# Kernel tuning notes

Hardware: AMD Instinct MI355X
Metric: run time of the kernel (lower is better)

Reference implementation:

```python
import jax, jax.numpy as jnp
import numpy as np

EPS = 1e-5

def _ln(x, g, b):
    mu = jnp.mean(x, axis=-1, keepdims=True)
    var = jnp.mean((x - mu) ** 2, axis=-1, keepdims=True)
    return (x - mu) * jax.lax.rsqrt(var + EPS) * g + b

def setup_inputs() -> dict:
    key = jax.random.key(0)
    B, V, I, H = 32, 48, 24, 768
    ks = jax.random.split(key, 10)
    s = 0.02
    return {
        'variables': jax.random.normal(ks[0], (B, V, H), jnp.float32),
        'interventions': jax.random.normal(ks[1], (B, I, H), jnp.float32),
        # variable_encoder: Linear(H,H) + LayerNorm(H)
        'W_enc': jax.random.normal(ks[2], (H, H), jnp.float32) * s,
        'b_enc': jnp.zeros((H,), jnp.float32),
        'g_enc': jnp.ones((H,), jnp.float32),
        'be_enc': jnp.zeros((H,), jnp.float32),
        # graph_generator: Linear(2H,H) + LN(H) + ReLU + Linear(H,1) + Sigmoid
        'Wg1': jax.random.normal(ks[3], (2 * H, H), jnp.float32) * s,
        'bg1': jnp.zeros((H,), jnp.float32),
        'g_g': jnp.ones((H,), jnp.float32),
        'b_g': jnp.zeros((H,), jnp.float32),
        'Wg2': jax.random.normal(ks[4], (H, 1), jnp.float32) * s,
        'bg2': jnp.zeros((1,), jnp.float32),
        # intervention_predictor: Linear(2H,H) + LN(H) + ReLU + Linear(H,H)
        'Wi1': jax.random.normal(ks[5], (2 * H, H), jnp.float32) * s,
        'bi1': jnp.zeros((H,), jnp.float32),
        'g_i': jnp.ones((H,), jnp.float32),
        'b_i': jnp.zeros((H,), jnp.float32),
        'Wi2': jax.random.normal(ks[6], (H, H), jnp.float32) * s,
        'bi2': jnp.zeros((H,), jnp.float32),
    }

def reference(variables, interventions, W_enc, b_enc, g_enc, be_enc,
              Wg1, bg1, g_g, b_g, Wg2, bg2, Wi1, bi1, g_i, b_i, Wi2, bi2):
    H = variables.shape[-1]
    V = variables.shape[1]
    # variable encoder: Linear + LayerNorm + ReLU
    enc = jax.nn.relu(_ln(variables @ W_enc + b_enc, g_enc, be_enc))  # [B,V,H]

    # graph generator over all ordered pairs (i,j): concat([enc_i, enc_j]) @ Wg1
    # split Wg1 so the concat-matmul becomes two small GEMMs + broadcast add
    hi = jnp.einsum('bvh,hk->bvk', enc, Wg1[:H])   # contribution of enc_i
    hj = jnp.einsum('bvh,hk->bvk', enc, Wg1[H:])   # contribution of enc_j
    h = jax.nn.relu(_ln(hi[:, :, None, :] + hj[:, None, :, :] + bg1, g_g, b_g))  # [B,V,V,H]
    score = jax.nn.sigmoid(jnp.squeeze(h @ Wg2, -1) + bg2[0])  # [B,V,V]
    # diagonal (i==j) is never written in the original -> stays zero
    causal_graph = score * (1.0 - jnp.eye(V, dtype=score.dtype))

    # intervention predictor: concat([intervention_i, enc_j]) -> MLP
    ha = jnp.einsum('bih,hk->bik', interventions, Wi1[:H])  # [B,I,H]
    hb = jnp.einsum('bvh,hk->bvk', enc, Wi1[H:])            # [B,V,H]
    h2 = jax.nn.relu(_ln(ha[:, :, None, :] + hb[:, None, :, :] + bi1, g_i, b_i))  # [B,I,V,H]
    effects = h2 @ Wi2 + bi2  # [B,I,V,H]

    return (effects, causal_graph, enc)
```

## Files before the change

kernel.cpp:

```cpp
#include <hip/hip_runtime.h>
#include <math.h>

#define Bp 32
#define Vp 48
#define Ip 24
#define Hp 768
#define EPS 1e-5f

#define EFFECTS_SIZE (Bp*Ip*Vp*Hp)
#define GRAPH_SIZE   (Bp*Vp*Vp)
#define ENC_SIZE     (Bp*Vp*Hp)
#define MS           (Hp*Hp)

typedef __attribute__((ext_vector_type(8))) short short8;
typedef __attribute__((ext_vector_type(4))) float floatx4;
typedef __attribute__((ext_vector_type(2))) float floatx2;
typedef __attribute__((ext_vector_type(4))) unsigned int uintx4;

__device__ __forceinline__ unsigned short f2bf(float f) {
    unsigned int u = __float_as_uint(f);
    u += 0x7fffu + ((u >> 16) & 1u);
    return (unsigned short)(u >> 16);
}
__device__ __forceinline__ unsigned int f2bf2(float a, float b) {
    return (unsigned int)f2bf(a) | ((unsigned int)f2bf(b) << 16);
}

__device__ __forceinline__ uintx4 ln8(floatx4 xa, floatx4 xb, float mu, float rs,
                                      floatx4 ga, floatx4 gb, floatx4 ba, floatx4 bb)
{
    float y0 = fmaxf((xa.x - mu) * rs * ga.x + ba.x, 0.f);
    float y1 = fmaxf((xa.y - mu) * rs * ga.y + ba.y, 0.f);
    float y2 = fmaxf((xa.z - mu) * rs * ga.z + ba.z, 0.f);
    float y3 = fmaxf((xa.w - mu) * rs * ga.w + ba.w, 0.f);
    float y4 = fmaxf((xb.x - mu) * rs * gb.x + bb.x, 0.f);
    float y5 = fmaxf((xb.y - mu) * rs * gb.y + bb.y, 0.f);
    float y6 = fmaxf((xb.z - mu) * rs * gb.z + bb.z, 0.f);
    float y7 = fmaxf((xb.w - mu) * rs * gb.w + bb.w, 0.f);
    uintx4 v;
    v.x = f2bf2(y0, y1); v.y = f2bf2(y2, y3);
    v.z = f2bf2(y4, y5); v.w = f2bf2(y6, y7);
    return v;
}

__global__ __launch_bounds__(256) void pack_weights(
    const float* __restrict__ W_enc, const float* __restrict__ Wg1,
    const float* __restrict__ Wi1, const float* __restrict__ Wi2,
    unsigned short* __restrict__ packed)
{
    const int bid = blockIdx.x;
    const int m = bid / 288;
    const int rem = bid - m * 288;
    const int T = rem / 6;
    const int u = rem - T * 6;
    const float* src;
    switch (m) {
        case 0: src = W_enc; break;
        case 1: src = Wg1; break;
        case 2: src = Wg1 + Hp * Hp; break;
        case 3: src = Wi1 + Hp * Hp; break;
        case 4: src = Wi1; break;
        default: src = Wi2; break;
    }
    unsigned short* dst = packed + (size_t)m * MS;
    const int lane = threadIdx.x & 63;
    const int kq = threadIdx.x >> 6;
    const int col = T * 16 + (lane & 15);
    const int krow0 = (lane >> 4) * 8;
    const int kb = kq + 4 * u;
    unsigned int w[4];
#pragma unroll
    for (int p2 = 0; p2 < 4; ++p2) {
        float f0 = src[(size_t)(kb * 32 + krow0 + 2 * p2)     * Hp + col];
        float f1 = src[(size_t)(kb * 32 + krow0 + 2 * p2 + 1) * Hp + col];
        w[p2] = f2bf2(f0, f1);
    }
    uintx4 v; v.x = w[0]; v.y = w[1]; v.z = w[2]; v.w = w[3];
    *(uintx4*)(dst + ((size_t)(T * 24 + kb) * 64 + lane) * 8) = v;
}

__global__ __launch_bounds__(256) void convert_inputs(
    const float* __restrict__ vars, const float* __restrict__ intv,
    const float* __restrict__ bg1, const float* __restrict__ bi1,
    unsigned short* __restrict__ varb, unsigned short* __restrict__ intvb,
    float* __restrict__ bias2304)
{
    const int p = blockIdx.x * 256 + threadIdx.x;
    const int VPn = ENC_SIZE / 2;
    if (p < VPn) {
        float2 f = ((const float2*)vars)[p];
        ((unsigned int*)varb)[p] = f2bf2(f.x, f.y);
    } else {
        int q = p - VPn;
        float2 f = ((const float2*)intv)[q];
        ((unsigned int*)intvb)[q] = f2bf2(f.x, f.y);
    }
    if (blockIdx.x == 0) {
        for (int t = threadIdx.x; t < 2304; t += 256)
            bias2304[t] = (t < 768) ? 0.0f : (t < 1536 ? bg1[t - 768] : bi1[t - 1536]);
    }
}

__device__ __forceinline__ void gemm32_body(
    unsigned short* Asl,
    const unsigned short* __restrict__ A, const unsigned short* __restrict__ Bpk,
    const float* __restrict__ bias, float* __restrict__ C, int ldc,
    int bx, int by)
{
    const int tid = threadIdx.x, wave = tid >> 6, lane = tid & 63;
    const int m0 = bx * 32;

#pragma unroll
    for (int uu = 0; uu < 12; ++uu) {
        const int s = tid + 256 * uu;
        const int mt = s / 1536;
        const int r2 = s - mt * 1536;
        const int kb = r2 >> 6;
        const int L  = r2 & 63;
        uintx4 v = *(const uintx4*)(A + (size_t)(m0 + mt * 16 + (L & 15)) * Hp
                                      + kb * 32 + (L >> 4) * 8);
        *(uintx4*)(&Asl[((mt * 24 + kb) * 64 + (L ^ (kb & 7))) * 8]) = v;
    }
    __syncthreads();

    const int mrow = lane & 15, kq = lane >> 4;
    const int rot = ((bx * 5 + by) & 7) * 3;
    const int wavep = (wave + bx) & 3;
    const int Tg0 = by * 12 + wavep * 3;
    const unsigned short* Bbase = Bpk + (size_t)Tg0 * 12288 + lane * 8;

    const floatx4 z = {0.f, 0.f, 0.f, 0.f};
    floatx4 acc[2][3];
#pragma unroll
    for (int mt = 0; mt < 2; ++mt)
#pragma unroll
        for (int nt = 0; nt < 3; ++nt) acc[mt][nt] = z;

    short8 bbuf[4][3], abuf[2][2];
#pragma unroll
    for (int d = 0; d < 3; ++d) {
        int kc = d + rot; if (kc >= 24) kc -= 24;
#pragma unroll
        for (int nt = 0; nt < 3; ++nt)
            bbuf[d][nt] = *(const short8*)(Bbase + (size_t)nt * 12288 + kc * 512);
    }
    {
        int kc = rot;
#pragma unroll
        for (int mt = 0; mt < 2; ++mt)
            abuf[0][mt] = *(const short8*)(&Asl[((mt * 24 + kc) * 64 + (lane ^ (kc & 7))) * 8]);
    }

#pragma unroll
    for (int kb = 0; kb < 24; ++kb) {
        if (kb + 3 < 24) {
            int kc = kb + 3 + rot; if (kc >= 24) kc -= 24;
#pragma unroll
            for (int nt = 0; nt < 3; ++nt)
                bbuf[(kb + 3) & 3][nt] =
                    *(const short8*)(Bbase + (size_t)nt * 12288 + kc * 512);
        }
        if (kb + 1 < 24) {
            int kc = kb + 1 + rot; if (kc >= 24) kc -= 24;
#pragma unroll
            for (int mt = 0; mt < 2; ++mt)
                abuf[(kb + 1) & 1][mt] = *(const short8*)(
                    &Asl[((mt * 24 + kc) * 64 + (lane ^ (kc & 7))) * 8]);
        }
        __builtin_amdgcn_s_setprio(1);
#pragma unroll
        for (int mt = 0; mt < 2; ++mt)
#pragma unroll
            for (int nt = 0; nt < 3; ++nt)
                acc[mt][nt] = __builtin_amdgcn_mfma_f32_16x16x32_bf16(
                    abuf[kb & 1][mt], bbuf[kb & 3][nt], acc[mt][nt], 0, 0, 0);
        __builtin_amdgcn_s_setprio(0);
    }

#pragma unroll
    for (int nt = 0; nt < 3; ++nt) {
        const int colg = (Tg0 + nt) * 16 + mrow;
        const float bv = bias ? bias[colg] : 0.0f;
#pragma unroll
        for (int mt = 0; mt < 2; ++mt)
#pragma unroll
            for (int r = 0; r < 4; ++r)
                C[(size_t)(m0 + mt * 16 + kq * 4 + r) * ldc + colg] = acc[mt][nt][r] + bv;
    }
}

__global__ __launch_bounds__(256) void gemm32(
    const unsigned short* __restrict__ A, const unsigned short* __restrict__ Bpk,
    const float* __restrict__ bias, float* __restrict__ C, int ldc)
{
    __shared__ unsigned short Asl[2 * 24 * 64 * 8];
    gemm32_body(Asl, A, Bpk, bias, C, ldc, blockIdx.x, blockIdx.y);
}

__global__ __launch_bounds__(256) void gemm32_pair(
    const unsigned short* __restrict__ A1, const unsigned short* __restrict__ B1,
    const float* __restrict__ bias1, float* __restrict__ C1,
    const unsigned short* __restrict__ A2, const unsigned short* __restrict__ B2,
    float* __restrict__ C2)
{
    __shared__ unsigned short Asl[2 * 24 * 64 * 8];
    if (blockIdx.y < 4) {
        gemm32_body(Asl, A1, B1, bias1, C1, Hp, blockIdx.x, blockIdx.y);
    } else {
        if (blockIdx.x >= 24) return;
        gemm32_body(Asl, A2, B2, nullptr, C2, Hp, blockIdx.x, blockIdx.y - 4);
    }
}

__global__ __launch_bounds__(256) void ln_relu(
    const float* __restrict__ pre, const float* __restrict__ g,
    const float* __restrict__ be, float* __restrict__ encf,
    unsigned short* __restrict__ encb)
{
    const int wave = threadIdx.x >> 6, lane = threadIdx.x & 63;
    const int row = blockIdx.x * 4 + wave;
    const float2* rp = (const float2*)(pre + (size_t)row * Hp);
    float2 x[6]; float s = 0.f, q = 0.f;
#pragma unroll
    for (int c = 0; c < 6; ++c) {
        x[c] = rp[lane + 64 * c];
        s += x[c].x + x[c].y;
        q += x[c].x * x[c].x + x[c].y * x[c].y;
    }
#pragma unroll
    for (int m = 1; m < 64; m <<= 1) { s += __shfl_xor(s, m, 64); q += __shfl_xor(q, m, 64); }
    const float mu = s * (1.0f / Hp);
    const float var = q * (1.0f / Hp) - mu * mu;
    const float rs = rsqrtf(var + EPS);
    floatx2* of = (floatx2*)(encf + (size_t)row * Hp);
    unsigned int* ob = (unsigned int*)(encb + (size_t)row * Hp);
#pragma unroll
    for (int c = 0; c < 6; ++c) {
        const float2 g2 = ((const float2*)g)[lane + 64 * c];
        const float2 b2 = ((const float2*)be)[lane + 64 * c];
        float y0 = fmaxf((x[c].x - mu) * rs * g2.x + b2.x, 0.f);
        float y1 = fmaxf((x[c].y - mu) * rs * g2.y + b2.y, 0.f);
        floatx2 y; y.x = y0; y.y = y1;
        __builtin_nontemporal_store(y, &of[lane + 64 * c]);
        ob[lane + 64 * c] = f2bf2(y0, y1);
    }
}

__global__ __launch_bounds__(384) void graph_v2(
    const float* __restrict__ ws2, const float* __restrict__ gg_,
    const float* __restrict__ bb_, const float* __restrict__ Wg2,
    const float* __restrict__ bg2, float* __restrict__ out)
{
    __shared__ floatx4 HJ[96 * 64];
    __shared__ floatx4 HI[6 * 192];
    __shared__ floatx4 Gc[192];
    __shared__ floatx4 Bc[192];
    __shared__ floatx4 W2c[192];
    const int tid = threadIdx.x, wave = tid >> 6, lane = tid & 63;
    const int b = blockIdx.x >> 3, ig = blockIdx.x & 7;
    const floatx4* w4 = (const floatx4*)ws2;

    for (int idx = tid; idx < 6 * 192; idx += 384) {
        const int i = idx / 192, c = idx - i * 192;
        HI[idx] = w4[(size_t)(b * 48 + ig * 6 + i) * 576 + c];
    }
    for (int c = tid; c < 192; c += 384) {
        Gc[c]  = ((const floatx4*)gg_)[c];
        Bc[c]  = ((const floatx4*)bb_)[c];
        W2c[c] = ((const floatx4*)Wg2)[c];
    }
    for (int idx = tid; idx < 48 * 96; idx += 384) {
        const int j = idx / 96, c = idx - j * 96;
        HJ[c * 64 + (j ^ (c & 7))] = w4[(size_t)(b * 48 + j) * 576 + 192 + c];
    }
    __syncthreads();

    float s = 0.f, q = 0.f, pd = 0.f, mu = 0.f, rs = 0.f;

    if (lane < 48) {
#pragma unroll 4
        for (int c = 0; c < 96; ++c) {
            const floatx4 x = HI[wave * 192 + c] + HJ[c * 64 + (lane ^ (c & 7))];
            s += x.x + x.y + x.z + x.w;
            q += x.x * x.x + x.y * x.y + x.z * x.z + x.w * x.w;
        }
    }
    __syncthreads();
    for (int idx = tid; idx < 48 * 96; idx += 384) {
        const int j = idx / 96, c = idx - j * 96;
        HJ[c * 64 + (j ^ (c & 7))] = w4[(size_t)(b * 48 + j) * 576 + 192 + 96 + c];
    }
    __syncthreads();

    if (lane < 48) {
#pragma unroll 4
        for (int c = 0; c < 96; ++c) {
            const floatx4 x = HI[wave * 192 + 96 + c] + HJ[c * 64 + (lane ^ (c & 7))];
            s += x.x + x.y + x.z + x.w;
            q += x.x * x.x + x.y * x.y + x.z * x.z + x.w * x.w;
        }
        mu = s * (1.0f / Hp);
        rs = rsqrtf(q * (1.0f / Hp) - mu * mu + EPS);
#pragma unroll 2
        for (int c = 0; c < 96; ++c) {
            const floatx4 x = HI[wave * 192 + 96 + c] + HJ[c * 64 + (lane ^ (c & 7))];
            const floatx4 g = Gc[96 + c], b2 = Bc[96 + c], w = W2c[96 + c];
            pd += fmaxf((x.x - mu) * rs * g.x + b2.x, 0.f) * w.x;
            pd += fmaxf((x.y - mu) * rs * g.y + b2.y, 0.f) * w.y;
            pd += fmaxf((x.z - mu) * rs * g.z + b2.z, 0.f) * w.z;
            pd += fmaxf((x.w - mu) * rs * g.w + b2.w, 0.f) * w.w;
        }
    }
    __syncthreads();
    for (int idx = tid; idx < 48 * 96; idx += 384) {
        const int j = idx / 96, c = idx - j * 96;
        HJ[c * 64 + (j ^ (c & 7))] = w4[(size_t)(b * 48 + j) * 576 + 192 + c];
    }
    __syncthreads();

    if (lane < 48) {
#pragma unroll 2
        for (int c = 0; c < 96; ++c) {
            const floatx4 x = HI[wave * 192 + c] + HJ[c * 64 + (lane ^ (c & 7))];
            const floatx4 g = Gc[c], b2 = Bc[c], w = W2c[c];
            pd += fmaxf((x.x - mu) * rs * g.x + b2.x, 0.f) * w.x;
            pd += fmaxf((x.y - mu) * rs * g.y + b2.y, 0.f) * w.y;
            pd += fmaxf((x.z - mu) * rs * g.z + b2.z, 0.f) * w.z;
            pd += fmaxf((x.w - mu) * rs * g.w + b2.w, 0.f) * w.w;
        }
        const int ii = ig * 6 + wave;
        const float v = pd + bg2[0];
        const float sc = (ii == lane) ? 0.f : 1.f / (1.f + expf(-v));
        out[((size_t)b * 48 + ii) * 48 + lane] = sc;
    }
}

__global__ __launch_bounds__(512, 2) void effects96(
    const float* __restrict__ ha, const float* __restrict__ ws2,
    const float* __restrict__ g_i, const float* __restrict__ b_i,
    const unsigned short* __restrict__ Bpk, const float* __restrict__ bi2,
    float* __restrict__ out)
{
    __shared__ unsigned short Asl[6 * 24 * 64 * 8];
    const int tid = threadIdx.x, wave = tid >> 6, lane = tid & 63;
    const int bid = blockIdx.x;
    const int pair = bid >> 1, nhalf = bid & 1;
    const int b = pair / 12;
    const int bi0 = b * Ip + (pair - b * 12) * 2;
    const int half = lane >> 5, hl = lane & 31;

    {
        const floatx4* ha0 = (const floatx4*)(ha + (size_t)bi0 * Hp);
        const floatx4* ha1 = (const floatx4*)(ha + (size_t)(bi0 + 1) * Hp);
        const floatx4* gp = (const floatx4*)g_i;
        const floatx4* bp = (const floatx4*)b_i;
        floatx4 hv0[6], hv1[6], gv[6], bv[6];
#pragma unroll
        for (int t = 0; t < 3; ++t) {
            hv0[2*t] = ha0[2*hl + 64*t];  hv0[2*t+1] = ha0[2*hl + 1 + 64*t];
            hv1[2*t] = ha1[2*hl + 64*t];  hv1[2*t+1] = ha1[2*hl + 1 + 64*t];
            gv[2*t]  = gp[2*hl + 64*t];   gv[2*t+1]  = gp[2*hl + 1 + 64*t];
            bv[2*t]  = bp[2*hl + 64*t];   bv[2*t+1]  = bp[2*hl + 1 + 64*t];
        }

#pragma unroll
        for (int p = 0; p < 3; ++p) {
            const int j = wave * 6 + 2 * p + half;
            const floatx4* hbp = (const floatx4*)(ws2 + (size_t)(b * Vp + j) * 2304 + 1536);
            floatx4 x0[6], x1[6];
            float s0 = 0.f, q0 = 0.f, s1 = 0.f, q1 = 0.f;
#pragma unroll
            for (int t = 0; t < 3; ++t) {
                const floatx4 hA = hbp[2*hl + 64*t];
                const floatx4 hB = hbp[2*hl + 1 + 64*t];
                x0[2*t]   = hv0[2*t]   + hA;  x0[2*t+1] = hv0[2*t+1] + hB;
                x1[2*t]   = hv1[2*t]   + hA;  x1[2*t+1] = hv1[2*t+1] + hB;
            }
#pragma unroll
            for (int c = 0; c < 6; ++c) {
                s0 += x0[c].x + x0[c].y + x0[c].z + x0[c].w;
                q0 += x0[c].x*x0[c].x + x0[c].y*x0[c].y + x0[c].z*x0[c].z + x0[c].w*x0[c].w;
                s1 += x1[c].x + x1[c].y + x1[c].z + x1[c].w;
                q1 += x1[c].x*x1[c].x + x1[c].y*x1[c].y + x1[c].z*x1[c].z + x1[c].w*x1[c].w;
            }
#pragma unroll
            for (int m = 1; m < 32; m <<= 1) {
                s0 += __shfl_xor(s0, m, 64); q0 += __shfl_xor(q0, m, 64);
                s1 += __shfl_xor(s1, m, 64); q1 += __shfl_xor(q1, m, 64);
            }
            const float mu0 = s0 * (1.0f / Hp);
            const float rs0 = rsqrtf(q0 * (1.0f / Hp) - mu0 * mu0 + EPS);
            const float mu1 = s1 * (1.0f / Hp);
            const float rs1 = rsqrtf(q1 * (1.0f / Hp) - mu1 * mu1 + EPS);
            const int mt0 = j >> 4, mt1 = 3 + mt0, mr = j & 15;
#pragma unroll
            for (int t = 0; t < 3; ++t) {
                const int cpk = hl + 32 * t;
                const int kb = cpk >> 2, kq2 = cpk & 3;
                const int swz = (kq2 * 16 + mr) ^ (kb & 7);
                uintx4 v0 = ln8(x0[2*t], x0[2*t+1], mu0, rs0,
                                gv[2*t], gv[2*t+1], bv[2*t], bv[2*t+1]);
                *(uintx4*)(&Asl[((mt0 * 24 + kb) * 64 + swz) * 8]) = v0;
                uintx4 v1 = ln8(x1[2*t], x1[2*t+1], mu1, rs1,
                                gv[2*t], gv[2*t+1], bv[2*t], bv[2*t+1]);
                *(uintx4*)(&Asl[((mt1 * 24 + kb) * 64 + swz) * 8]) = v1;
            }
        }
    }
    __syncthreads();

    const int mrow = lane & 15, kq = lane >> 4;
    const int rot = (pair & 7) * 3;
    const int wavep = (wave + pair) & 7;
    const int Tg0 = nhalf * 24 + wavep * 3;
    const unsigned short* Bbase = Bpk + (size_t)Tg0 * 12288 + lane * 8;

    const floatx4 z = {0.f, 0.f, 0.f, 0.f};
    floatx4 acc[6][3];
#pragma unroll
    for (int mt = 0; mt < 6; ++mt)
#pragma unroll
        for (int nt = 0; nt < 3; ++nt) acc[mt][nt] = z;

    short8 bbuf[4][3], abuf[2][6];
#pragma unroll
    for (int d = 0; d < 3; ++d) {
        int kc = d + rot; if (kc >= 24) kc -= 24;
#pragma unroll
        for (int nt = 0; nt < 3; ++nt)
            bbuf[d][nt] = *(const short8*)(Bbase + (size_t)nt * 12288 + kc * 512);
    }
    {
        int kc = rot;
#pragma unroll
        for (int mt = 0; mt < 6; ++mt)
            abuf[0][mt] = *(const short8*)(&Asl[((mt * 24 + kc) * 64 + (lane ^ (kc & 7))) * 8]);
    }

#pragma unroll
    for (int kb = 0; kb < 24; ++kb) {
        if (kb + 3 < 24) {
            int kc = kb + 3 + rot; if (kc >= 24) kc -= 24;
#pragma unroll
            for (int nt = 0; nt < 3; ++nt)
                bbuf[(kb + 3) & 3][nt] =
                    *(const short8*)(Bbase + (size_t)nt * 12288 + kc * 512);
        }
        if (kb + 1 < 24) {
            int kc = kb + 1 + rot; if (kc >= 24) kc -= 24;
#pragma unroll
            for (int mt = 0; mt < 6; ++mt)
                abuf[(kb + 1) & 1][mt] = *(const short8*)(
                    &Asl[((mt * 24 + kc) * 64 + (lane ^ (kc & 7))) * 8]);
        }
        __builtin_amdgcn_s_setprio(1);
#pragma unroll
        for (int mt = 0; mt < 6; ++mt)
#pragma unroll
            for (int nt = 0; nt < 3; ++nt)
                acc[mt][nt] = __builtin_amdgcn_mfma_f32_16x16x32_bf16(
                    abuf[kb & 1][mt], bbuf[kb & 3][nt], acc[mt][nt], 0, 0, 0);
        __builtin_amdgcn_s_setprio(0);
    }

#pragma unroll
    for (int nt = 0; nt < 3; ++nt) {
        const int colg = (Tg0 + nt) * 16 + mrow;
        const float biasv = bi2[colg];
#pragma unroll
        for (int mt = 0; mt < 6; ++mt) {
#pragma unroll
            for (int r = 0; r < 4; ++r) {
                const int rr = mt * 16 + kq * 4 + r;
                __builtin_nontemporal_store(
                    acc[mt][nt][r] + biasv,
                    &out[(size_t)(bi0 * 48 + rr) * Hp + colg]);
            }
        }
    }
}

extern "C" void kernel_launch(void* const* d_in, const int* in_sizes, int n_in,
                              void* d_out, int out_size, void* d_ws, size_t ws_size,
                              hipStream_t stream) {
    const float* variables     = (const float*)d_in[0];
    const float* interventions = (const float*)d_in[1];
    const float* W_enc  = (const float*)d_in[2];
    const float* b_enc  = (const float*)d_in[3];
    const float* g_enc  = (const float*)d_in[4];
    const float* be_enc = (const float*)d_in[5];
    const float* Wg1 = (const float*)d_in[6];
    const float* bg1 = (const float*)d_in[7];
    const float* g_g = (const float*)d_in[8];
    const float* b_g = (const float*)d_in[9];
    const float* Wg2 = (const float*)d_in[10];
    const float* bg2 = (const float*)d_in[11];
    const float* Wi1 = (const float*)d_in[12];
    const float* bi1 = (const float*)d_in[13];
    const float* g_i = (const float*)d_in[14];
    const float* b_i = (const float*)d_in[15];
    const float* Wi2 = (const float*)d_in[16];
    const float* bi2 = (const float*)d_in[17];

    float* out = (float*)d_out;
    float* effects = out;
    float* graph = out + EFFECTS_SIZE;
    float* enc_f = out + EFFECTS_SIZE + GRAPH_SIZE;

    char* wsb = (char*)d_ws;
    unsigned short* packedW = (unsigned short*)wsb;
    float* ws2  = (float*)(wsb + 7077888);
    float* pre1 = ws2;
    float* ha   = (float*)(wsb + 7077888 + 14155776);
    unsigned short* varb  = (unsigned short*)(wsb + 23592960);
    unsigned short* intvb = (unsigned short*)(wsb + 25952256);
    unsigned short* encb  = (unsigned short*)(wsb + 27131904);
    float* bias2304 = (float*)(wsb + 29491200);

    pack_weights<<<1728, 256, 0, stream>>>(W_enc, Wg1, Wi1, Wi2, packedW);
    convert_inputs<<<3456, 256, 0, stream>>>(variables, interventions, bg1, bi1,
                                             varb, intvb, bias2304);
    gemm32_pair<<<dim3(48, 8), 256, 0, stream>>>(varb, packedW, b_enc, pre1,
                                                 intvb, packedW + (size_t)4 * MS, ha);
    ln_relu<<<384, 256, 0, stream>>>(pre1, g_enc, be_enc, enc_f, encb);
    gemm32<<<dim3(48, 12), 256, 0, stream>>>(encb, packedW + (size_t)1 * MS,
                                             bias2304, ws2, 2304);
    graph_v2<<<256, 384, 0, stream>>>(ws2, g_g, b_g, Wg2, bg2, graph);
    effects96<<<768, 512, 0, stream>>>(ha, ws2, g_i, b_i,
                                       packedW + (size_t)5 * MS, bi2, effects);
}
```

Baseline: 298.5 us.

## Split fused encoder/intervention GEMM launch and preload hb rows in effects kernel

Removes the gemm32_pair kernel, which ran the encoder GEMM and the intervention GEMM as one launch, and runs them as separate gemm32 launches. The intervention GEMM now runs after the Wg1/Wi1 GEMM. In effects96, the three hb rows are loaded into registers up front before the LayerNorm loop, so the global loads are issued together. This adds a kernel launch and raises register pressure in effects96, but it simplifies the GEMM code and may improve load latency hiding.

After: 304.8 us. 1.02x slower.

```diff
diff --git a/kernel.cpp b/kernel.cpp
--- a/kernel.cpp
+++ b/kernel.cpp
@@ -101,14 +101,13 @@
     }
 }
 
-__device__ __forceinline__ void gemm32_body(
-    unsigned short* Asl,
+__global__ __launch_bounds__(256) void gemm32(
     const unsigned short* __restrict__ A, const unsigned short* __restrict__ Bpk,
-    const float* __restrict__ bias, float* __restrict__ C, int ldc,
-    int bx, int by)
-{
+    const float* __restrict__ bias, float* __restrict__ C, int ldc)
+{
+    __shared__ unsigned short Asl[2 * 24 * 64 * 8];
     const int tid = threadIdx.x, wave = tid >> 6, lane = tid & 63;
-    const int m0 = bx * 32;
+    const int m0 = blockIdx.x * 32;
 
 #pragma unroll
     for (int uu = 0; uu < 12; ++uu) {
@@ -124,9 +123,9 @@
     __syncthreads();
 
     const int mrow = lane & 15, kq = lane >> 4;
-    const int rot = ((bx * 5 + by) & 7) * 3;
-    const int wavep = (wave + bx) & 3;
-    const int Tg0 = by * 12 + wavep * 3;
+    const int rot = ((blockIdx.x * 5 + blockIdx.y) & 7) * 3;
+    const int wavep = (wave + blockIdx.x) & 3;
+    const int Tg0 = blockIdx.y * 12 + wavep * 3;
     const unsigned short* Bbase = Bpk + (size_t)Tg0 * 12288 + lane * 8;
 
     const floatx4 z = {0.f, 0.f, 0.f, 0.f};
@@ -186,29 +185,6 @@
 #pragma unroll
             for (int r = 0; r < 4; ++r)
                 C[(size_t)(m0 + mt * 16 + kq * 4 + r) * ldc + colg] = acc[mt][nt][r] + bv;
-    }
-}
-
-__global__ __launch_bounds__(256) void gemm32(
-    const unsigned short* __restrict__ A, const unsigned short* __restrict__ Bpk,
-    const float* __restrict__ bias, float* __restrict__ C, int ldc)
-{
-    __shared__ unsigned short Asl[2 * 24 * 64 * 8];
-    gemm32_body(Asl, A, Bpk, bias, C, ldc, blockIdx.x, blockIdx.y);
-}
-
-__global__ __launch_bounds__(256) void gemm32_pair(
-    const unsigned short* __restrict__ A1, const unsigned short* __restrict__ B1,
-    const float* __restrict__ bias1, float* __restrict__ C1,
-    const unsigned short* __restrict__ A2, const unsigned short* __restrict__ B2,
-    float* __restrict__ C2)
-{
-    __shared__ unsigned short Asl[2 * 24 * 64 * 8];
-    if (blockIdx.y < 4) {
-        gemm32_body(Asl, A1, B1, bias1, C1, Hp, blockIdx.x, blockIdx.y);
-    } else {
-        if (blockIdx.x >= 24) return;
-        gemm32_body(Asl, A2, B2, nullptr, C2, Hp, blockIdx.x, blockIdx.y - 4);
     }
 }
 
@@ -363,18 +339,27 @@
             bv[2*t]  = bp[2*hl + 64*t];   bv[2*t+1]  = bp[2*hl + 1 + 64*t];
         }
 
+        floatx4 hb[3][6];
 #pragma unroll
         for (int p = 0; p < 3; ++p) {
             const int j = wave * 6 + 2 * p + half;
             const floatx4* hbp = (const floatx4*)(ws2 + (size_t)(b * Vp + j) * 2304 + 1536);
+#pragma unroll
+            for (int t = 0; t < 3; ++t) {
+                hb[p][2*t]   = hbp[2*hl + 64*t];
+                hb[p][2*t+1] = hbp[2*hl + 1 + 64*t];
+            }
+        }
+
+#pragma unroll
+        for (int p = 0; p < 3; ++p) {
+            const int j = wave * 6 + 2 * p + half;
             floatx4 x0[6], x1[6];
             float s0 = 0.f, q0 = 0.f, s1 = 0.f, q1 = 0.f;
 #pragma unroll
-            for (int t = 0; t < 3; ++t) {
-                const floatx4 hA = hbp[2*hl + 64*t];
-                const floatx4 hB = hbp[2*hl + 1 + 64*t];
-                x0[2*t]   = hv0[2*t]   + hA;  x0[2*t+1] = hv0[2*t+1] + hB;
-                x1[2*t]   = hv1[2*t]   + hA;  x1[2*t+1] = hv1[2*t+1] + hB;
+            for (int c = 0; c < 6; ++c) {
+                x0[c] = hv0[c] + hb[p][c];
+                x1[c] = hv1[c] + hb[p][c];
             }
 #pragma unroll
             for (int c = 0; c < 6; ++c) {
@@ -520,11 +505,12 @@
     pack_weights<<<1728, 256, 0, stream>>>(W_enc, Wg1, Wi1, Wi2, packedW);
     convert_inputs<<<3456, 256, 0, stream>>>(variables, interventions, bg1, bi1,
                                              varb, intvb, bias2304);
-    gemm32_pair<<<dim3(48, 8), 256, 0, stream>>>(varb, packedW, b_enc, pre1,
-                                                 intvb, packedW + (size_t)4 * MS, ha);
+    gemm32<<<dim3(48, 4), 256, 0, stream>>>(varb, packedW, b_enc, pre1, Hp);
     ln_relu<<<384, 256, 0, stream>>>(pre1, g_enc, be_enc, enc_f, encb);
     gemm32<<<dim3(48, 12), 256, 0, stream>>>(encb, packedW + (size_t)1 * MS,
                                              bias2304, ws2, 2304);
+    gemm32<<<dim3(24, 4), 256, 0, stream>>>(intvb, packedW + (size_t)4 * MS,
+                                            nullptr, ha, Hp);
     graph_v2<<<256, 384, 0, stream>>>(ws2, g_g, b_g, Wg2, bg2, graph);
     effects96<<<768, 512, 0, stream>>>(ha, ws2, g_i, b_i,
                                        packedW + (size_t)5 * MS, bi2, effects);
```
